# Kernel tuning notes

Hardware: AMD Instinct MI355X
Metric: run time of the kernel (lower is better)

## Reference

```python
import jax, jax.numpy as jnp
import numpy as np
from jax import lax

B, D, H, W = 8, 256, 56, 56
DH = 32            # d_head
HEADS = D // DH    # 8
WIN = 7            # window size
TOPK = 8           # top-k windows
DM = 4 * D         # mlp hidden = 1024
EPS = 1e-5


def bn(x, g, b, m, v):
    # inference-mode BatchNorm2d over channel dim of NCHW
    return g[:, None, None] * (x - m[:, None, None]) * lax.rsqrt(v[:, None, None] + EPS) + b[:, None, None]


def conv1x1(x, w):
    return jnp.einsum('bchw,oc->bohw', x, w)


def setup_inputs() -> dict:
    key = jax.random.key(0)
    ks = jax.random.split(key, 24)
    s = 0.05
    return {
        'x': jax.random.normal(ks[0], (B, D, H, W), jnp.float32),
        'g1': jax.random.uniform(ks[1], (D,)) + 0.5,
        'b1': jax.random.normal(ks[2], (D,)) * s,
        'm1': jax.random.normal(ks[3], (D,)) * s,
        'v1': jax.random.uniform(ks[4], (D,)) + 0.5,
        'W_qkv': jax.random.normal(ks[5], (3 * D, D)) * s,
        'W_merge': jax.random.normal(ks[6], (D, D)) * s,
        'b_merge': jax.random.normal(ks[7], (D,)) * s,
        'W1': jax.random.normal(ks[8], (DM, D)) * s,
        'g2': jax.random.uniform(ks[9], (DM,)) + 0.5,
        'b2': jax.random.normal(ks[10], (DM,)) * s,
        'm2': jax.random.normal(ks[11], (DM,)) * s,
        'v2': jax.random.uniform(ks[12], (DM,)) + 0.5,
        'Wdw': jax.random.normal(ks[13], (DM, 1, 3, 3)) * s,
        'g3': jax.random.uniform(ks[14], (DM,)) + 0.5,
        'b3': jax.random.normal(ks[15], (DM,)) * s,
        'm3': jax.random.normal(ks[16], (DM,)) * s,
        'v3': jax.random.uniform(ks[17], (DM,)) + 0.5,
        'W2': jax.random.normal(ks[18], (D, DM)) * s,
        'g4': jax.random.uniform(ks[19], (D,)) + 0.5,
        'b4': jax.random.normal(ks[20], (D,)) * s,
        'm4': jax.random.normal(ks[21], (D,)) * s,
        'v4': jax.random.uniform(ks[22], (D,)) + 0.5,
    }


def _forward(x, g1, b1, m1, v1, W_qkv, W_merge, b_merge,
             W1, g2, b2, m2, v2, Wdw, g3, b3, m3, v3, W2, g4, b4, m4, v4):
    b_, d, Hh, Ww = x.shape
    nh, nw = Hh // WIN, Ww // WIN
    nWnd, ww = nh * nw, WIN * WIN

    # qkv projection: BN -> GELU -> 1x1 conv
    h = jax.nn.gelu(bn(x, g1, b1, m1, v1), approximate=False)
    qkv = conv1x1(h, W_qkv)
    q, k, v = jnp.split(qkv, 3, axis=1)  # each [b, d, H, W]

    def part(t):  # -> [b, heads, nWnd, ww, dh]
        t = t.reshape(b_, HEADS, DH, nh, WIN, nw, WIN)
        return jnp.transpose(t, (0, 1, 3, 5, 4, 6, 2)).reshape(b_, HEADS, nWnd, ww, DH)

    qw, kw, vw = part(q), part(k), part(v)

    # window-level routing: mean-pooled q/k per window, top-k window selection
    def pool(t):  # [b, d, H, W] -> [b, nWnd, d]
        t = t.reshape(b_, d, nh, WIN, nw, WIN).mean(axis=(3, 5))
        return t.reshape(b_, d, nWnd).transpose(0, 2, 1)

    qr, kr = pool(q), pool(k)
    aff = jnp.einsum('bnd,bmd->bnm', qr, kr)        # [b, nWnd, nWnd]
    idx = lax.top_k(aff, TOPK)[1]                    # [b, nWnd, TOPK]

    def gath(t, i):  # t [heads, nWnd, ww, dh], i [nWnd, TOPK]
        return t[:, i]  # [heads, nWnd, TOPK, ww, dh]

    kg = jax.vmap(gath)(kw, idx).reshape(b_, HEADS, nWnd, TOPK * ww, DH)
    vg = jax.vmap(gath)(vw, idx).reshape(b_, HEADS, nWnd, TOPK * ww, DH)

    scores = jnp.einsum('bhnqd,bhnkd->bhnqk', qw, kg) / jnp.sqrt(jnp.float32(DH))
    attn = jax.nn.softmax(scores, axis=-1)
    out = jnp.einsum('bhnqk,bhnkd->bhnqd', attn, vg)  # [b, heads, nWnd, ww, dh]

    # un-partition back to [b, d, H, W]
    out = out.reshape(b_, HEADS, nh, nw, WIN, WIN, DH)
    msg = jnp.transpose(out, (0, 1, 6, 2, 4, 3, 5)).reshape(b_, d, Hh, Ww)

    # merge (1x1 conv with bias) + residual
    x = x + conv1x1(msg, W_merge) + b_merge[None, :, None, None]

    # MB mlp block: 1x1 -> BN -> GELU -> dw3x3 -> BN -> GELU -> 1x1 -> BN
    h2 = conv1x1(x, W1)
    h2 = jax.nn.gelu(bn(h2, g2, b2, m2, v2), approximate=False)
    h2 = lax.conv_general_dilated(h2, Wdw, (1, 1), 'SAME',
                                  feature_group_count=DM,
                                  dimension_numbers=('NCHW', 'OIHW', 'NCHW'))
    h2 = jax.nn.gelu(bn(h2, g3, b3, m3, v3), approximate=False)
    h2 = conv1x1(h2, W2)
    h2 = bn(h2, g4, b4, m4, v4)
    return x + h2


def reference(x, g1, b1, m1, v1, W_qkv, W_merge, b_merge,
              W1, g2, b2, m2, v2, Wdw, g3, b3, m3, v3, W2, g4, b4, m4, v4):
    return _forward(x, g1, b1, m1, v1, W_qkv, W_merge, b_merge,
                    W1, g2, b2, m2, v2, Wdw, g3, b3, m3, v3, W2, g4, b4, m4, v4)
```

## Files before the change

### kernel.cpp

```cpp
#include <hip/hip_runtime.h>
#include <cstdint>
#include <cstddef>

#define BB 8
#define PP 3136
#define EPSV 1e-5f
#define SCQK 0.17677669529663687f

using bf16x8 = __attribute__((ext_vector_type(8))) short;
using f32x4  = __attribute__((ext_vector_type(4))) float;

__device__ __forceinline__ float bf2f(unsigned short u) {
    union { float f; unsigned int i; } c; c.i = ((unsigned int)u) << 16; return c.f;
}
__device__ __forceinline__ unsigned short f2bf(float f) {
    union { float f; unsigned int i; } c; c.f = f;
    unsigned int r = c.i + 0x7FFFu + ((c.i >> 16) & 1u);
    return (unsigned short)(r >> 16);
}
__device__ __forceinline__ float gelu_f(float t) {
    return 0.5f * t * (1.0f + erff(t * 0.70710678118654752440f));
}
__device__ __forceinline__ float gelu_fast(float x) {
    float z = 1.5957691216057308f * (x + 0.044715f * x * x * x);
    return x / (1.0f + __expf(-z));
}
__device__ __forceinline__ void async16(const void* g, void* s) {
    __builtin_amdgcn_global_load_lds(
        (const __attribute__((address_space(1))) unsigned int*)g,
        (__attribute__((address_space(3))) unsigned int*)s, 16, 0, 0);
}
__device__ __forceinline__ uint4 pack8(const float* v) {
    uint4 o;
    o.x = (unsigned)f2bf(v[0]) | ((unsigned)f2bf(v[1]) << 16);
    o.y = (unsigned)f2bf(v[2]) | ((unsigned)f2bf(v[3]) << 16);
    o.z = (unsigned)f2bf(v[4]) | ((unsigned)f2bf(v[5]) << 16);
    o.w = (unsigned)f2bf(v[6]) | ((unsigned)f2bf(v[7]) << 16);
    return o;
}

__global__ __launch_bounds__(256) void cvt_all_k(
    const float* __restrict__ Wq, const float* __restrict__ Wm,
    const float* __restrict__ W1, const float* __restrict__ W2,
    unsigned short* __restrict__ dq, unsigned short* __restrict__ dm,
    unsigned short* __restrict__ d1, unsigned short* __restrict__ d2)
{
    int i = blockIdx.x * 256 + threadIdx.x;
    if (i < 196608) dq[i] = f2bf(Wq[i]);
    else if (i < 262144) dm[i - 196608] = f2bf(Wm[i - 196608]);
    else if (i < 524288) d1[i - 262144] = f2bf(W1[i - 262144]);
    else d2[i - 524288] = f2bf(W2[i - 524288]);
}

__global__ __launch_bounds__(256) void transin_k(const float* __restrict__ x,
    const float* __restrict__ g1, const float* __restrict__ b1,
    const float* __restrict__ m1, const float* __restrict__ v1,
    float* __restrict__ x_pm, unsigned short* __restrict__ h_bf)
{
    __shared__ float tile[64][65];
    __shared__ float gam[64], bet[64], mu[64], rst[64];
    const int p0 = blockIdx.x * 64, c0 = blockIdx.y * 64, b = blockIdx.z;
    const int t = threadIdx.x;
    if (t < 64) { int c = c0 + t; gam[t] = g1[c]; bet[t] = b1[c]; mu[t] = m1[c]; rst[t] = rsqrtf(v1[c] + EPSV); }
    {
        int cl = t >> 2, px = (t & 3) * 16;
        const float* src = x + ((size_t)(b * 256 + c0 + cl)) * PP + p0 + px;
        #pragma unroll
        for (int i4 = 0; i4 < 4; i4++) {
            float4 r0 = *(const float4*)(src + i4 * 4);
            tile[cl][px + i4*4 + 0] = r0.x; tile[cl][px + i4*4 + 1] = r0.y;
            tile[cl][px + i4*4 + 2] = r0.z; tile[cl][px + i4*4 + 3] = r0.w;
        }
    }
    __syncthreads();
    {
        int pl = t >> 2, cb = (t & 3) * 16;
        float raw[16], hg[16];
        #pragma unroll
        for (int i = 0; i < 16; i++) {
            float vv = tile[cb + i][pl];
            raw[i] = vv;
            hg[i] = gelu_fast(gam[cb + i] * (vv - mu[cb + i]) * rst[cb + i] + bet[cb + i]);
        }
        size_t off = ((size_t)b * PP + p0 + pl) * 256 + c0 + cb;
        float* xd = x_pm + off;
        #pragma unroll
        for (int i4 = 0; i4 < 4; i4++) {
            float4 o; o.x = raw[i4*4]; o.y = raw[i4*4+1]; o.z = raw[i4*4+2]; o.w = raw[i4*4+3];
            *(float4*)(xd + i4 * 4) = o;
        }
        uint4* hd = (uint4*)(h_bf + off);
        hd[0] = pack8(&hg[0]);
        hd[1] = pack8(&hg[8]);
    }
}

template<int EPI>
__global__ __launch_bounds__(256) void gemm_mfma_k(
    const unsigned short* __restrict__ Aact,
    const unsigned short* __restrict__ Wbf,
    const int K, const int Mout,
    void* __restrict__ C1, void* __restrict__ C2,
    const float* __restrict__ e0, const float* __restrict__ e1,
    const float* __restrict__ e2, const float* __restrict__ e3,
    const float* __restrict__ resid)
{
    __shared__ __align__(16) char smem[34816];
    unsigned short* As0 = (unsigned short*)smem;
    unsigned short* Bs0 = (unsigned short*)(smem + 16384);
    float* T = (float*)smem;

    const int tid = threadIdx.x;
    const int w = tid >> 6, lane = tid & 63, g = lane >> 4, l15 = lane & 15;
    const int wm = w >> 1, wn = w & 1;
    const size_t row0 = (size_t)blockIdx.x * 128;
    const int n0 = blockIdx.y * 128;
    const int srow = tid >> 2, scb = tid & 3;

    const f32x4 vzero = {0.f, 0.f, 0.f, 0.f};
    f32x4 acc[4][4];
    #pragma unroll
    for (int mf = 0; mf < 4; mf++)
        #pragma unroll
        for (int nf = 0; nf < 4; nf++) acc[mf][nf] = vzero;

    const int NT = K >> 5;

    auto STAGE = [&](int s) {
        const int k0 = s << 5;
        unsigned short* Ad = As0 + (s & 1) * 4096;
        unsigned short* Bd = Bs0 + (s & 1) * 4096;
        #pragma unroll
        for (int r = 0; r < 2; r++) {
            int row = r * 64 + srow;
            int cbp = scb ^ ((row >> 1) & 3);
            async16(Aact + (row0 + row) * K + k0 + cbp * 8, Ad + r * 2048 + w * 512);
            async16(Wbf + (size_t)(n0 + row) * K + k0 + cbp * 8, Bd + r * 2048 + w * 512);
        }
    };
    auto COMPUTE = [&](int t) {
        const unsigned short* Ab = As0 + (t & 1) * 4096;
        const unsigned short* Bb = Bs0 + (t & 1) * 4096;
        bf16x8 af[4], bfr[4];
        #pragma unroll
        for (int mf = 0; mf < 4; mf++) {
            int row = wm * 64 + mf * 16 + l15;
            int gb = g ^ ((row >> 1) & 3);
            af[mf] = *(const bf16x8*)&Ab[row * 32 + gb * 8];
        }
        #pragma unroll
        for (int nf = 0; nf < 4; nf++) {
            int row = wn * 64 + nf * 16 + l15;
            int gb = g ^ ((row >> 1) & 3);
            bfr[nf] = *(const bf16x8*)&Bb[row * 32 + gb * 8];
        }
        #pragma unroll
        for (int mf = 0; mf < 4; mf++)
            #pragma unroll
            for (int nf = 0; nf < 4; nf++)
                acc[mf][nf] = __builtin_amdgcn_mfma_f32_16x16x32_bf16(af[mf], bfr[nf], acc[mf][nf], 0, 0, 0);
    };

    STAGE(0);
    for (int t = 0; t < NT; ++t) {
        __syncthreads();
        if (t + 1 < NT) STAGE(t + 1);
        COMPUTE(t);
    }

    __syncthreads();
    const int erow = tid >> 1;
    const int ec0 = (tid & 1) * 32;
    #pragma unroll
    for (int pass = 0; pass < 2; ++pass) {
        if (pass) __syncthreads();
        if (wn == pass) {
            #pragma unroll
            for (int mf = 0; mf < 4; mf++)
                #pragma unroll
                for (int nf = 0; nf < 4; nf++)
                    #pragma unroll
                    for (int r = 0; r < 4; r++)
                        T[(wm * 64 + mf * 16 + g * 4 + r) * 68 + nf * 16 + l15] = acc[mf][nf][r];
        }
        __syncthreads();
        float vals[32];
        #pragma unroll
        for (int i = 0; i < 8; i++) {
            float4 v = *(const float4*)&T[erow * 68 + ec0 + i * 4];
            vals[i*4+0] = v.x; vals[i*4+1] = v.y; vals[i*4+2] = v.z; vals[i*4+3] = v.w;
        }
        const size_t prow = row0 + erow;
        const int mc0 = n0 + pass * 64 + ec0;
        const size_t off = prow * Mout + mc0;
        if (EPI == 0) {
            const float s = (mc0 < 256) ? SCQK : 1.0f;
            #pragma unroll
            for (int j = 0; j < 32; j++) vals[j] *= s;
            uint4* dst = (uint4*)((unsigned short*)C1 + off);
            #pragma unroll
            for (int i = 0; i < 4; i++) dst[i] = pack8(&vals[i * 8]);
        } else if (EPI == 1) {
            #pragma unroll
            for (int i = 0; i < 8; i++) {
                float4 bi = *(const float4*)(e0 + mc0 + i * 4);
                float4 rr = *(const float4*)(resid + off + i * 4);
                vals[i*4+0] += bi.x + rr.x; vals[i*4+1] += bi.y + rr.y;
                vals[i*4+2] += bi.z + rr.z; vals[i*4+3] += bi.w + rr.w;
            }
            float4* d1 = (float4*)((float*)C1 + off);
            #pragma unroll
            for (int i = 0; i < 8; i++) {
                float4 o; o.x = vals[i*4]; o.y = vals[i*4+1]; o.z = vals[i*4+2]; o.w = vals[i*4+3];
                d1[i] = o;
            }
            uint4* d2 = (uint4*)((unsigned short*)C2 + off);
            #pragma unroll
            for (int i = 0; i < 4; i++) d2[i] = pack8(&vals[i * 8]);
        } else if (EPI == 2) {
            #pragma unroll
            for (int i = 0; i < 8; i++) {
                float4 ga = *(const float4*)(e0 + mc0 + i * 4);
                float4 be = *(const float4*)(e1 + mc0 + i * 4);
                float4 mm = *(const float4*)(e2 + mc0 + i * 4);
                float4 vv = *(const float4*)(e3 + mc0 + i * 4);
                vals[i*4+0] = gelu_fast(ga.x * (vals[i*4+0] - mm.x) * rsqrtf(vv.x + EPSV) + be.x);
                vals[i*4+1] = gelu_fast(ga.y * (vals[i*4+1] - mm.y) * rsqrtf(vv.y + EPSV) + be.y);
                vals[i*4+2] = gelu_fast(ga.z * (vals[i*4+2] - mm.z) * rsqrtf(vv.z + EPSV) + be.z);
                vals[i*4+3] = gelu_fast(ga.w * (vals[i*4+3] - mm.w) * rsqrtf(vv.w + EPSV) + be.w);
            }
            uint4* dst = (uint4*)((unsigned short*)C1 + off);
            #pragma unroll
            for (int i = 0; i < 4; i++) dst[i] = pack8(&vals[i * 8]);
        } else {
            #pragma unroll
            for (int i = 0; i < 8; i++) {
                float4 ga = *(const float4*)(e0 + mc0 + i * 4);
                float4 be = *(const float4*)(e1 + mc0 + i * 4);
                float4 mm = *(const float4*)(e2 + mc0 + i * 4);
                float4 vv = *(const float4*)(e3 + mc0 + i * 4);
                float4 rr = *(const float4*)(resid + off + i * 4);
                vals[i*4+0] = ga.x * (vals[i*4+0] - mm.x) * rsqrtf(vv.x + EPSV) + be.x + rr.x;
                vals[i*4+1] = ga.y * (vals[i*4+1] - mm.y) * rsqrtf(vv.y + EPSV) + be.y + rr.y;
                vals[i*4+2] = ga.z * (vals[i*4+2] - mm.z) * rsqrtf(vv.z + EPSV) + be.z + rr.z;
                vals[i*4+3] = ga.w * (vals[i*4+3] - mm.w) * rsqrtf(vv.w + EPSV) + be.w + rr.w;
            }
            float4* d1 = (float4*)((float*)C1 + off);
            #pragma unroll
            for (int i = 0; i < 8; i++) {
                float4 o; o.x = vals[i*4]; o.y = vals[i*4+1]; o.z = vals[i*4+2]; o.w = vals[i*4+3];
                d1[i] = o;
            }
        }
    }
}

__global__ __launch_bounds__(256) void poolh_k(const float* __restrict__ x_pm,
    const float* __restrict__ g1, const float* __restrict__ b1,
    const float* __restrict__ m1, const float* __restrict__ v1,
    float* __restrict__ ph)
{
    __shared__ float part[4][256];
    __shared__ float gam[256], bet[256], mu[256], rst[256];
    const int n = blockIdx.x, b = blockIdx.y, t = threadIdx.x;
    gam[t] = g1[t]; bet[t] = b1[t]; mu[t] = m1[t]; rst[t] = rsqrtf(v1[t] + EPSV);
    __syncthreads();
    const int c4 = (t & 63) * 4, pg = t >> 6;
    float s0 = 0.f, s1 = 0.f, s2 = 0.f, s3 = 0.f;
    for (int j = pg; j < 49; j += 4) {
        int p = ((n >> 3) * 7 + j / 7) * 56 + (n & 7) * 7 + j % 7;
        float4 vx = *(const float4*)(x_pm + ((size_t)b * PP + p) * 256 + c4);
        s0 += gelu_f(gam[c4+0] * (vx.x - mu[c4+0]) * rst[c4+0] + bet[c4+0]);
        s1 += gelu_f(gam[c4+1] * (vx.y - mu[c4+1]) * rst[c4+1] + bet[c4+1]);
        s2 += gelu_f(gam[c4+2] * (vx.z - mu[c4+2]) * rst[c4+2] + bet[c4+2]);
        s3 += gelu_f(gam[c4+3] * (vx.w - mu[c4+3]) * rst[c4+3] + bet[c4+3]);
    }
    part[pg][c4 + 0] = s0; part[pg][c4 + 1] = s1; part[pg][c4 + 2] = s2; part[pg][c4 + 3] = s3;
    __syncthreads();
    float tot = part[0][t] + part[1][t] + part[2][t] + part[3][t];
    ph[((size_t)b * 64 + n) * 256 + t] = tot * (1.0f / 49.0f);
}

__global__ __launch_bounds__(256) void qrkr_k(const float* __restrict__ ph,
    const float* __restrict__ Wqkv, float* __restrict__ qr, float* __restrict__ kr)
{
    __shared__ float row[256];
    const int n = blockIdx.x, b = blockIdx.y, t = threadIdx.x;
    row[t] = ph[((size_t)b * 64 + n) * 256 + t];
    __syncthreads();
    const float* wq = Wqkv + (size_t)t * 256;
    const float* wk = Wqkv + (size_t)(256 + t) * 256;
    float aq = 0.f, ak = 0.f;
    #pragma unroll 4
    for (int k = 0; k < 256; k += 4) {
        float4 a4 = *(const float4*)(wq + k);
        float4 b4 = *(const float4*)(wk + k);
        aq += row[k]*a4.x + row[k+1]*a4.y + row[k+2]*a4.z + row[k+3]*a4.w;
        ak += row[k]*b4.x + row[k+1]*b4.y + row[k+2]*b4.z + row[k+3]*b4.w;
    }
    qr[((size_t)b * 64 + n) * 256 + t] = aq;
    kr[((size_t)b * 64 + n) * 256 + t] = ak;
}

__global__ __launch_bounds__(64) void topk_k(const float* __restrict__ qr,
    const float* __restrict__ kr, int* __restrict__ idxb)
{
    const int n = blockIdx.x, b_ = blockIdx.y;
    const int tid = threadIdx.x;
    __shared__ float qrow[256];
    *reinterpret_cast<float4*>(&qrow[tid * 4]) =
        *reinterpret_cast<const float4*>(qr + ((size_t)(b_ * 64) + n) * 256 + tid * 4);
    __syncthreads();
    const float* kp = kr + ((size_t)(b_ * 64) + tid) * 256;
    float av = 0.f;
    #pragma unroll 4
    for (int c = 0; c < 256; c++) av = fmaf(qrow[c], kp[c], av);
    for (int t = 0; t < 8; t++) {
        float v = av; int id = tid;
        #pragma unroll
        for (int off = 32; off; off >>= 1) {
            float v2 = __shfl_xor(v, off);
            int id2 = __shfl_xor(id, off);
            if (v2 > v || (v2 == v && id2 < id)) { v = v2; id = id2; }
        }
        if (tid == 0) idxb[((b_ * 64) + n) * 8 + t] = id;
        if (tid == id) av = -1e30f;
    }
}

__global__ __launch_bounds__(256) void attn_mfma_k(const unsigned short* __restrict__ qkv,
    const int* __restrict__ idxb, unsigned short* __restrict__ msg)
{
    __shared__ __align__(16) unsigned short Ks[64 * 40];
    __shared__ __align__(16) unsigned short Vt[32 * 72];
    __shared__ __align__(16) unsigned short Pr[4][16 * 72];
    const int n = blockIdx.x, h = blockIdx.y, b = blockIdx.z;
    const int tid = threadIdx.x;
    const int w = tid >> 6, lane = tid & 63, g = lane >> 4, l15 = lane & 15;

    for (int e = tid; e < 64 * 40; e += 256) Ks[e] = 0;
    for (int e = tid; e < 32 * 72; e += 256) Vt[e] = 0;

    const int iq = w * 16 + l15;
    bf16x8 qf = {0, 0, 0, 0, 0, 0, 0, 0};
    if (iq < 49) {
        int p = ((n >> 3) * 7 + iq / 7) * 56 + (n & 7) * 7 + iq % 7;
        qf = *(const bf16x8*)(qkv + ((size_t)b * PP + p) * 768 + h * 32 + g * 8);
    }
    const f32x4 vzero = {0.f, 0.f, 0.f, 0.f};
    f32x4 o0 = vzero, o1 = vzero;
    float mrow = -1e30f, lrow = 0.f;

    const bool act = tid < 196;
    const int jrow = tid >> 2, c8 = (tid & 3) * 8;
    uint4 kk_r = {0,0,0,0}, vv_r = {0,0,0,0};
    auto LOADW = [&](int t) {
        int wsrc = idxb[((b * 64) + n) * 8 + t];
        int p = ((wsrc >> 3) * 7 + jrow / 7) * 56 + (wsrc & 7) * 7 + jrow % 7;
        const unsigned short* srcp = qkv + ((size_t)b * PP + p) * 768 + 256 + h * 32 + c8;
        kk_r = *(const uint4*)srcp;
        vv_r = *(const uint4*)(srcp + 256);
    };
    if (act) LOADW(0);

    for (int t = 0; t < 8; t++) {
        __syncthreads();
        if (act) {
            *(uint4*)&Ks[jrow * 40 + c8] = kk_r;
            const unsigned short* pv = (const unsigned short*)&vv_r;
            #pragma unroll
            for (int jj = 0; jj < 8; jj++) {
                int dh = c8 + jj;
                Vt[dh * 72 + (jrow ^ (((dh >> 3) & 3) << 3))] = pv[jj];
            }
            if (t < 7) LOADW(t + 1);
        }
        __syncthreads();
        f32x4 s[4];
        #pragma unroll
        for (int nf = 0; nf < 4; nf++) {
            bf16x8 kf = *(const bf16x8*)&Ks[(nf * 16 + l15) * 40 + g * 8];
            s[nf] = __builtin_amdgcn_mfma_f32_16x16x32_bf16(kf, qf, vzero, 0, 0, 0);
        }
        float sv[16];
        #pragma unroll
        for (int nf = 0; nf < 4; nf++)
            #pragma unroll
            for (int r = 0; r < 4; r++) {
                int j = nf * 16 + g * 4 + r;
                sv[nf * 4 + r] = (j < 49) ? s[nf][r] : -1e30f;
            }
        float wmx = sv[0];
        #pragma unroll
        for (int e = 1; e < 16; e++) wmx = fmaxf(wmx, sv[e]);
        wmx = fmaxf(wmx, __shfl_xor(wmx, 16));
        wmx = fmaxf(wmx, __shfl_xor(wmx, 32));
        float mn = fmaxf(mrow, wmx);
        float corr = __expf(mrow - mn);
        mrow = mn;
        float rsum = 0.f;
        #pragma unroll
        for (int e = 0; e < 16; e++) { float pe = __expf(sv[e] - mn); sv[e] = pe; rsum += pe; }
        rsum += __shfl_xor(rsum, 16);
        rsum += __shfl_xor(rsum, 32);
        lrow = lrow * corr + rsum;
        #pragma unroll
        for (int r = 0; r < 4; r++) { o0[r] *= corr; o1[r] *= corr; }
        #pragma unroll
        for (int nf = 0; nf < 4; nf++) {
            uint2 pw;
            pw.x = (unsigned)f2bf(sv[nf*4+0]) | ((unsigned)f2bf(sv[nf*4+1]) << 16);
            pw.y = (unsigned)f2bf(sv[nf*4+2]) | ((unsigned)f2bf(sv[nf*4+3]) << 16);
            *(uint2*)&Pr[w][l15 * 72 + nf * 16 + g * 4] = pw;
        }
        asm volatile("s_waitcnt lgkmcnt(0)" ::: "memory");
        #pragma unroll
        for (int ks = 0; ks < 2; ks++) {
            const int j0 = ks * 32 + g * 8;
            bf16x8 pf  = *(const bf16x8*)&Pr[w][l15 * 72 + j0];
            bf16x8 vf0 = *(const bf16x8*)&Vt[l15 * 72 + (j0 ^ (((l15 >> 3) & 1) << 3))];
            bf16x8 vf1 = *(const bf16x8*)&Vt[(16 + l15) * 72 + (j0 ^ ((2 + (l15 >> 3)) << 3))];
            o0 = __builtin_amdgcn_mfma_f32_16x16x32_bf16(vf0, pf, o0, 0, 0, 0);
            o1 = __builtin_amdgcn_mfma_f32_16x16x32_bf16(vf1, pf, o1, 0, 0, 0);
        }
    }
    if (iq < 49) {
        float inv = 1.0f / lrow;
        int p = ((n >> 3) * 7 + iq / 7) * 56 + (n & 7) * 7 + iq % 7;
        size_t off = ((size_t)b * PP + p) * 256 + h * 32;
        uint2 w0, w1;
        w0.x = (unsigned)f2bf(o0[0]*inv) | ((unsigned)f2bf(o0[1]*inv) << 16);
        w0.y = (unsigned)f2bf(o0[2]*inv) | ((unsigned)f2bf(o0[3]*inv) << 16);
        w1.x = (unsigned)f2bf(o1[0]*inv) | ((unsigned)f2bf(o1[1]*inv) << 16);
        w1.y = (unsigned)f2bf(o1[2]*inv) | ((unsigned)f2bf(o1[3]*inv) << 16);
        *(uint2*)(msg + off + g * 4) = w0;
        *(uint2*)(msg + off + 16 + g * 4) = w1;
    }
}

__global__ __launch_bounds__(256) void dwconv_k(const unsigned short* __restrict__ in,
    const float* __restrict__ w9,
    const float* __restrict__ g3, const float* __restrict__ b3,
    const float* __restrict__ m3, const float* __restrict__ v3,
    unsigned short* __restrict__ out)
{
    __shared__ __align__(16) unsigned short tl[100 * 64];
    const int sx = blockIdx.x % 7, sy = blockIdx.x / 7;
    const int c0 = blockIdx.y * 64, b = blockIdx.z;
    const int t = threadIdx.x;
    for (int e = t; e < 800; e += 256) {
        int pos = e >> 3, c8 = (e & 7) * 8;
        int iy = sy * 8 + pos / 10 - 1, ix = sx * 8 + pos % 10 - 1;
        uint4 val = {0u, 0u, 0u, 0u};
        if (iy >= 0 && iy < 56 && ix >= 0 && ix < 56)
            val = *(const uint4*)(in + ((size_t)b * PP + iy * 56 + ix) * 1024 + c0 + c8);
        *(uint4*)&tl[pos * 64 + c8] = val;
    }
    __syncthreads();
    const int c2 = (t & 31) * 2, pg = t >> 5;
    const int c = c0 + c2;
    float w0[9], w1[9];
    #pragma unroll
    for (int i = 0; i < 9; i++) { w0[i] = w9[c * 9 + i]; w1[i] = w9[(c + 1) * 9 + i]; }
    const float ga0 = g3[c], be0 = b3[c], mu0 = m3[c], rs0 = rsqrtf(v3[c] + EPSV);
    const float ga1 = g3[c+1], be1 = b3[c+1], mu1 = m3[c+1], rs1 = rsqrtf(v3[c+1] + EPSV);
    #pragma unroll
    for (int q = 0; q < 8; q++) {
        int pos = pg * 8 + q, y = pos >> 3, xq = pos & 7;
        float s0 = 0.f, s1 = 0.f;
        #pragma unroll
        for (int dy = 0; dy < 3; dy++)
            #pragma unroll
            for (int dx = 0; dx < 3; dx++) {
                unsigned int u = *(const unsigned int*)&tl[((y + dy) * 10 + xq + dx) * 64 + c2];
                s0 = fmaf(bf2f((unsigned short)(u & 0xffffu)), w0[dy * 3 + dx], s0);
                s1 = fmaf(bf2f((unsigned short)(u >> 16)), w1[dy * 3 + dx], s1);
            }
        float y0 = gelu_fast(ga0 * (s0 - mu0) * rs0 + be0);
        float y1 = gelu_fast(ga1 * (s1 - mu1) * rs1 + be1);
        unsigned int ow = (unsigned int)f2bf(y0) | ((unsigned int)f2bf(y1) << 16);
        size_t off = ((size_t)b * PP + (sy * 8 + y) * 56 + sx * 8 + xq) * 1024 + c;
        *(unsigned int*)&out[off] = ow;
    }
}

__global__ __launch_bounds__(256) void transout_k(const float* __restrict__ out_pm,
    float* __restrict__ dout)
{
    __shared__ float tile[64][65];
    const int p0 = blockIdx.x * 64, c0 = blockIdx.y * 64, b = blockIdx.z;
    const int t = threadIdx.x;
    {
        int pl = t >> 2, cx = (t & 3) * 16;
        const float* src = out_pm + ((size_t)b * PP + p0 + pl) * 256 + c0 + cx;
        #pragma unroll
        for (int i4 = 0; i4 < 4; i4++) {
            float4 vv = *(const float4*)(src + i4 * 4);
            tile[pl][cx + i4*4 + 0] = vv.x; tile[pl][cx + i4*4 + 1] = vv.y;
            tile[pl][cx + i4*4 + 2] = vv.z; tile[pl][cx + i4*4 + 3] = vv.w;
        }
    }
    __syncthreads();
    {
        int cl = t >> 2, px = (t & 3) * 16;
        float* dst = dout + ((size_t)(b * 256 + c0 + cl)) * PP + p0 + px;
        #pragma unroll
        for (int i4 = 0; i4 < 4; i4++) {
            float4 o;
            o.x = tile[px + i4*4 + 0][cl]; o.y = tile[px + i4*4 + 1][cl];
            o.z = tile[px + i4*4 + 2][cl]; o.w = tile[px + i4*4 + 3][cl];
            *(float4*)(dst + i4 * 4) = o;
        }
    }
}

extern "C" void kernel_launch(void* const* d_in, const int* in_sizes, int n_in,
                              void* d_out, int out_size, void* d_ws, size_t ws_size,
                              hipStream_t stream)
{
    const float* x      = (const float*)d_in[0];
    const float* g1     = (const float*)d_in[1];
    const float* b1     = (const float*)d_in[2];
    const float* m1     = (const float*)d_in[3];
    const float* v1     = (const float*)d_in[4];
    const float* Wqkv   = (const float*)d_in[5];
    const float* Wmerge = (const float*)d_in[6];
    const float* bmerge = (const float*)d_in[7];
    const float* W1     = (const float*)d_in[8];
    const float* g2     = (const float*)d_in[9];
    const float* b2     = (const float*)d_in[10];
    const float* m2     = (const float*)d_in[11];
    const float* v2     = (const float*)d_in[12];
    const float* Wdw    = (const float*)d_in[13];
    const float* g3     = (const float*)d_in[14];
    const float* b3     = (const float*)d_in[15];
    const float* m3     = (const float*)d_in[16];
    const float* v3     = (const float*)d_in[17];
    const float* W2     = (const float*)d_in[18];
    const float* g4     = (const float*)d_in[19];
    const float* b4     = (const float*)d_in[20];
    const float* m4     = (const float*)d_in[21];
    const float* v4     = (const float*)d_in[22];

    char* ws = (char*)d_ws;
    float*          x_pm   = (float*)(ws + 0);
    float*          x2_pm  = (float*)(ws + 25690112);
    unsigned short* x2_bf  = (unsigned short*)(ws + 51380224);
    unsigned short* qkv_pm = (unsigned short*)(ws + 64225280);
    unsigned short* msg_pm = (unsigned short*)(ws + 102760448);
    unsigned short* t1     = (unsigned short*)(ws + 115605504);
    unsigned short* h_bf   = t1;
    unsigned short* t2     = (unsigned short*)(ws + 166985728);
    float*          ph     = (float*)(ws + 218365952);
    float*          qr     = (float*)(ws + 218890240);
    float*          kr     = (float*)(ws + 219414528);
    int*            idxb   = (int*)(ws + 219938816);
    unsigned short* Wqkv_b = (unsigned short*)(ws + 219955200);
    unsigned short* Wmrg_b = (unsigned short*)(ws + 220348416);
    unsigned short* W1_b   = (unsigned short*)(ws + 220479488);
    unsigned short* W2_b   = (unsigned short*)(ws + 221003776);
    float*          out_pm = x_pm;
    if (ws_size < 221528064) return;

    cvt_all_k<<<3072, 256, 0, stream>>>(Wqkv, Wmerge, W1, W2, Wqkv_b, Wmrg_b, W1_b, W2_b);
    transin_k<<<dim3(49, 4, BB), 256, 0, stream>>>(x, g1, b1, m1, v1, x_pm, h_bf);
    gemm_mfma_k<0><<<dim3(196, 6), 256, 0, stream>>>(h_bf, Wqkv_b, 256, 768,
        qkv_pm, nullptr, nullptr, nullptr, nullptr, nullptr, nullptr);
    poolh_k<<<dim3(64, BB), 256, 0, stream>>>(x_pm, g1, b1, m1, v1, ph);
    qrkr_k<<<dim3(64, BB), 256, 0, stream>>>(ph, Wqkv, qr, kr);
    topk_k<<<dim3(64, BB), 64, 0, stream>>>(qr, kr, idxb);
    attn_mfma_k<<<dim3(64, 8, BB), 256, 0, stream>>>(qkv_pm, idxb, msg_pm);
    gemm_mfma_k<1><<<dim3(196, 2), 256, 0, stream>>>(msg_pm, Wmrg_b, 256, 256,
        x2_pm, x2_bf, bmerge, nullptr, nullptr, nullptr, x_pm);
    gemm_mfma_k<2><<<dim3(196, 8), 256, 0, stream>>>(x2_bf, W1_b, 256, 1024,
        t1, nullptr, g2, b2, m2, v2, nullptr);
    dwconv_k<<<dim3(49, 16, BB), 256, 0, stream>>>(t1, Wdw, g3, b3, m3, v3, t2);
    gemm_mfma_k<3><<<dim3(196, 2), 256, 0, stream>>>(t2, W2_b, 1024, 256,
        out_pm, nullptr, g4, b4, m4, v4, x2_pm);
    transout_k<<<dim3(49, 4, BB), 256, 0, stream>>>(out_pm, (float*)d_out);
}
```

Before: 340.9 us.

## Restructure GEMM to stream A from global, stage weights in LDS; load K directly

```diff
diff --git a/kernel.cpp b/kernel.cpp
--- a/kernel.cpp
+++ b/kernel.cpp
@@ -105,104 +105,97 @@
     const float* __restrict__ e2, const float* __restrict__ e3,
     const float* __restrict__ resid)
 {
-    __shared__ __align__(16) char smem[34816];
-    unsigned short* As0 = (unsigned short*)smem;
-    unsigned short* Bs0 = (unsigned short*)(smem + 16384);
+    __shared__ __align__(16) char smem[32768];
+    unsigned short* Bs = (unsigned short*)smem;
     float* T = (float*)smem;
 
     const int tid = threadIdx.x;
     const int w = tid >> 6, lane = tid & 63, g = lane >> 4, l15 = lane & 15;
     const int wm = w >> 1, wn = w & 1;
     const size_t row0 = (size_t)blockIdx.x * 128;
-    const int n0 = blockIdx.y * 128;
-    const int srow = tid >> 2, scb = tid & 3;
+    const int n0 = blockIdx.y * 64;
 
     const f32x4 vzero = {0.f, 0.f, 0.f, 0.f};
-    f32x4 acc[4][4];
+    f32x4 acc[4][2];
     #pragma unroll
     for (int mf = 0; mf < 4; mf++)
         #pragma unroll
-        for (int nf = 0; nf < 4; nf++) acc[mf][nf] = vzero;
-
-    const int NT = K >> 5;
-
-    auto STAGE = [&](int s) {
-        const int k0 = s << 5;
-        unsigned short* Ad = As0 + (s & 1) * 4096;
-        unsigned short* Bd = Bs0 + (s & 1) * 4096;
-        #pragma unroll
-        for (int r = 0; r < 2; r++) {
-            int row = r * 64 + srow;
-            int cbp = scb ^ ((row >> 1) & 3);
-            async16(Aact + (row0 + row) * K + k0 + cbp * 8, Ad + r * 2048 + w * 512);
-            async16(Wbf + (size_t)(n0 + row) * K + k0 + cbp * 8, Bd + r * 2048 + w * 512);
-        }
-    };
-    auto COMPUTE = [&](int t) {
-        const unsigned short* Ab = As0 + (t & 1) * 4096;
-        const unsigned short* Bb = Bs0 + (t & 1) * 4096;
-        bf16x8 af[4], bfr[4];
-        #pragma unroll
-        for (int mf = 0; mf < 4; mf++) {
-            int row = wm * 64 + mf * 16 + l15;
-            int gb = g ^ ((row >> 1) & 3);
-            af[mf] = *(const bf16x8*)&Ab[row * 32 + gb * 8];
-        }
-        #pragma unroll
-        for (int nf = 0; nf < 4; nf++) {
-            int row = wn * 64 + nf * 16 + l15;
-            int gb = g ^ ((row >> 1) & 3);
-            bfr[nf] = *(const bf16x8*)&Bb[row * 32 + gb * 8];
-        }
-        #pragma unroll
-        for (int mf = 0; mf < 4; mf++)
-            #pragma unroll
-            for (int nf = 0; nf < 4; nf++)
-                acc[mf][nf] = __builtin_amdgcn_mfma_f32_16x16x32_bf16(af[mf], bfr[nf], acc[mf][nf], 0, 0, 0);
-    };
-
-    STAGE(0);
-    for (int t = 0; t < NT; ++t) {
+        for (int nf = 0; nf < 2; nf++) acc[mf][nf] = vzero;
+
+    const int nchunk = K >> 8;
+    const unsigned short* Arow[4];
+    #pragma unroll
+    for (int mf = 0; mf < 4; mf++)
+        Arow[mf] = Aact + (row0 + wm * 64 + mf * 16 + l15) * (size_t)K + g * 8;
+
+    for (int c = 0; c < nchunk; ++c) {
+        if (c) __syncthreads();
+        #pragma unroll
+        for (int rd = 0; rd < 8; rd++) {
+            int idx = rd * 256 + tid;
+            int brow = idx >> 5;
+            int bcb  = idx & 31;
+            int bcbs = bcb ^ (brow & 15);
+            unsigned short* dst = Bs + ((rd * 256 + (tid & ~63)) << 3);
+            async16(Wbf + ((size_t)(n0 + brow)) * K + c * 256 + bcbs * 8, dst);
+        }
         __syncthreads();
-        if (t + 1 < NT) STAGE(t + 1);
-        COMPUTE(t);
-    }
-
-    __syncthreads();
-    const int erow = tid >> 1;
-    const int ec0 = (tid & 1) * 32;
-    #pragma unroll
-    for (int pass = 0; pass < 2; ++pass) {
-        if (pass) __syncthreads();
-        if (wn == pass) {
+        const int kc = c << 8;
+        #pragma unroll
+        for (int ks = 0; ks < 8; ks++) {
+            bf16x8 af[4];
+            #pragma unroll
+            for (int mf = 0; mf < 4; mf++)
+                af[mf] = *(const bf16x8*)(Arow[mf] + kc + ks * 32);
+            bf16x8 bfr[2];
+            #pragma unroll
+            for (int nf = 0; nf < 2; nf++) {
+                int brow = wn * 32 + nf * 16 + l15;
+                int bcb = (ks * 4 + g) ^ (brow & 15);
+                bfr[nf] = *(const bf16x8*)&Bs[brow * 256 + bcb * 8];
+            }
             #pragma unroll
             for (int mf = 0; mf < 4; mf++)
                 #pragma unroll
-                for (int nf = 0; nf < 4; nf++)
+                for (int nf = 0; nf < 2; nf++)
+                    acc[mf][nf] = __builtin_amdgcn_mfma_f32_16x16x32_bf16(af[mf], bfr[nf], acc[mf][nf], 0, 0, 0);
+        }
+    }
+
+    __syncthreads();
+    const int erow = tid >> 2;
+    const int ec0 = (tid & 3) * 16;
+    #pragma unroll
+    for (int half = 0; half < 2; ++half) {
+        if (half) __syncthreads();
+        if (wm == half) {
+            #pragma unroll
+            for (int mf = 0; mf < 4; mf++)
+                #pragma unroll
+                for (int nf = 0; nf < 2; nf++)
                     #pragma unroll
                     for (int r = 0; r < 4; r++)
-                        T[(wm * 64 + mf * 16 + g * 4 + r) * 68 + nf * 16 + l15] = acc[mf][nf][r];
+                        T[(mf * 16 + g * 4 + r) * 68 + wn * 32 + nf * 16 + l15] = acc[mf][nf][r];
         }
         __syncthreads();
-        float vals[32];
-        #pragma unroll
-        for (int i = 0; i < 8; i++) {
+        float vals[16];
+        #pragma unroll
+        for (int i = 0; i < 4; i++) {
             float4 v = *(const float4*)&T[erow * 68 + ec0 + i * 4];
             vals[i*4+0] = v.x; vals[i*4+1] = v.y; vals[i*4+2] = v.z; vals[i*4+3] = v.w;
         }
-        const size_t prow = row0 + erow;
-        const int mc0 = n0 + pass * 64 + ec0;
+        const size_t prow = row0 + half * 64 + erow;
+        const int mc0 = n0 + ec0;
         const size_t off = prow * Mout + mc0;
         if (EPI == 0) {
             const float s = (mc0 < 256) ? SCQK : 1.0f;
             #pragma unroll
-            for (int j = 0; j < 32; j++) vals[j] *= s;
+            for (int j = 0; j < 16; j++) vals[j] *= s;
             uint4* dst = (uint4*)((unsigned short*)C1 + off);
-            #pragma unroll
-            for (int i = 0; i < 4; i++) dst[i] = pack8(&vals[i * 8]);
+            dst[0] = pack8(&vals[0]); dst[1] = pack8(&vals[8]);
         } else if (EPI == 1) {
             #pragma unroll
-            for (int i = 0; i < 8; i++) {
+            for (int i = 0; i < 4; i++) {
                 float4 bi = *(const float4*)(e0 + mc0 + i * 4);
                 float4 rr = *(const float4*)(resid + off + i * 4);
                 vals[i*4+0] += bi.x + rr.x; vals[i*4+1] += bi.y + rr.y;
@@ -210,16 +203,15 @@
             }
             float4* d1 = (float4*)((float*)C1 + off);
             #pragma unroll
-            for (int i = 0; i < 8; i++) {
+            for (int i = 0; i < 4; i++) {
                 float4 o; o.x = vals[i*4]; o.y = vals[i*4+1]; o.z = vals[i*4+2]; o.w = vals[i*4+3];
                 d1[i] = o;
             }
             uint4* d2 = (uint4*)((unsigned short*)C2 + off);
-            #pragma unroll
-            for (int i = 0; i < 4; i++) d2[i] = pack8(&vals[i * 8]);
+            d2[0] = pack8(&vals[0]); d2[1] = pack8(&vals[8]);
         } else if (EPI == 2) {
             #pragma unroll
-            for (int i = 0; i < 8; i++) {
+            for (int i = 0; i < 4; i++) {
                 float4 ga = *(const float4*)(e0 + mc0 + i * 4);
                 float4 be = *(const float4*)(e1 + mc0 + i * 4);
                 float4 mm = *(const float4*)(e2 + mc0 + i * 4);
@@ -230,11 +222,10 @@
                 vals[i*4+3] = gelu_fast(ga.w * (vals[i*4+3] - mm.w) * rsqrtf(vv.w + EPSV) + be.w);
             }
             uint4* dst = (uint4*)((unsigned short*)C1 + off);
-            #pragma unroll
-            for (int i = 0; i < 4; i++) dst[i] = pack8(&vals[i * 8]);
+            dst[0] = pack8(&vals[0]); dst[1] = pack8(&vals[8]);
         } else {
             #pragma unroll
-            for (int i = 0; i < 8; i++) {
+            for (int i = 0; i < 4; i++) {
                 float4 ga = *(const float4*)(e0 + mc0 + i * 4);
                 float4 be = *(const float4*)(e1 + mc0 + i * 4);
                 float4 mm = *(const float4*)(e2 + mc0 + i * 4);
@@ -247,7 +238,7 @@
             }
             float4* d1 = (float4*)((float*)C1 + off);
             #pragma unroll
-            for (int i = 0; i < 8; i++) {
+            for (int i = 0; i < 4; i++) {
                 float4 o; o.x = vals[i*4]; o.y = vals[i*4+1]; o.z = vals[i*4+2]; o.w = vals[i*4+3];
                 d1[i] = o;
             }
@@ -331,14 +322,12 @@
 __global__ __launch_bounds__(256) void attn_mfma_k(const unsigned short* __restrict__ qkv,
     const int* __restrict__ idxb, unsigned short* __restrict__ msg)
 {
-    __shared__ __align__(16) unsigned short Ks[64 * 40];
     __shared__ __align__(16) unsigned short Vt[32 * 72];
     __shared__ __align__(16) unsigned short Pr[4][16 * 72];
     const int n = blockIdx.x, h = blockIdx.y, b = blockIdx.z;
     const int tid = threadIdx.x;
     const int w = tid >> 6, lane = tid & 63, g = lane >> 4, l15 = lane & 15;
 
-    for (int e = tid; e < 64 * 40; e += 256) Ks[e] = 0;
     for (int e = tid; e < 32 * 72; e += 256) Vt[e] = 0;
 
     const int iq = w * 16 + l15;
@@ -347,41 +336,52 @@
         int p = ((n >> 3) * 7 + iq / 7) * 56 + (n & 7) * 7 + iq % 7;
         qf = *(const bf16x8*)(qkv + ((size_t)b * PP + p) * 768 + h * 32 + g * 8);
     }
+    int widx[8];
+    {
+        const int* ip = idxb + ((b * 64) + n) * 8;
+        #pragma unroll
+        for (int t = 0; t < 8; t++) widx[t] = ip[t];
+    }
     const f32x4 vzero = {0.f, 0.f, 0.f, 0.f};
     f32x4 o0 = vzero, o1 = vzero;
     float mrow = -1e30f, lrow = 0.f;
 
     const bool act = tid < 196;
     const int jrow = tid >> 2, c8 = (tid & 3) * 8;
-    uint4 kk_r = {0,0,0,0}, vv_r = {0,0,0,0};
-    auto LOADW = [&](int t) {
-        int wsrc = idxb[((b * 64) + n) * 8 + t];
+    uint4 vv_r = {0,0,0,0};
+    auto LOADV = [&](int t) {
+        int wsrc = widx[t];
         int p = ((wsrc >> 3) * 7 + jrow / 7) * 56 + (wsrc & 7) * 7 + jrow % 7;
-        const unsigned short* srcp = qkv + ((size_t)b * PP + p) * 768 + 256 + h * 32 + c8;
-        kk_r = *(const uint4*)srcp;
-        vv_r = *(const uint4*)(srcp + 256);
+        vv_r = *(const uint4*)(qkv + ((size_t)b * PP + p) * 768 + 512 + h * 32 + c8);
     };
-    if (act) LOADW(0);
+    if (act) LOADV(0);
 
     for (int t = 0; t < 8; t++) {
+        const int wsrc = widx[t];
+        const int sy0 = (wsrc >> 3) * 7, sx0 = (wsrc & 7) * 7;
+        bf16x8 kf[4];
+        #pragma unroll
+        for (int nf = 0; nf < 4; nf++) {
+            int j = nf * 16 + l15;
+            int jc = (j < 49) ? j : 0;
+            int p = (sy0 + jc / 7) * 56 + sx0 + jc % 7;
+            kf[nf] = *(const bf16x8*)(qkv + ((size_t)b * PP + p) * 768 + 256 + h * 32 + g * 8);
+        }
         __syncthreads();
         if (act) {
-            *(uint4*)&Ks[jrow * 40 + c8] = kk_r;
             const unsigned short* pv = (const unsigned short*)&vv_r;
             #pragma unroll
             for (int jj = 0; jj < 8; jj++) {
                 int dh = c8 + jj;
                 Vt[dh * 72 + (jrow ^ (((dh >> 3) & 3) << 3))] = pv[jj];
             }
-            if (t < 7) LOADW(t + 1);
+            if (t < 7) LOADV(t + 1);
         }
         __syncthreads();
         f32x4 s[4];
         #pragma unroll
-        for (int nf = 0; nf < 4; nf++) {
-            bf16x8 kf = *(const bf16x8*)&Ks[(nf * 16 + l15) * 40 + g * 8];
-            s[nf] = __builtin_amdgcn_mfma_f32_16x16x32_bf16(kf, qf, vzero, 0, 0, 0);
-        }
+        for (int nf = 0; nf < 4; nf++)
+            s[nf] = __builtin_amdgcn_mfma_f32_16x16x32_bf16(kf[nf], qf, vzero, 0, 0, 0);
         float sv[16];
         #pragma unroll
         for (int nf = 0; nf < 4; nf++)
@@ -564,18 +564,18 @@
 
     cvt_all_k<<<3072, 256, 0, stream>>>(Wqkv, Wmerge, W1, W2, Wqkv_b, Wmrg_b, W1_b, W2_b);
     transin_k<<<dim3(49, 4, BB), 256, 0, stream>>>(x, g1, b1, m1, v1, x_pm, h_bf);
-    gemm_mfma_k<0><<<dim3(196, 6), 256, 0, stream>>>(h_bf, Wqkv_b, 256, 768,
+    gemm_mfma_k<0><<<dim3(196, 12), 256, 0, stream>>>(h_bf, Wqkv_b, 256, 768,
         qkv_pm, nullptr, nullptr, nullptr, nullptr, nullptr, nullptr);
     poolh_k<<<dim3(64, BB), 256, 0, stream>>>(x_pm, g1, b1, m1, v1, ph);
     qrkr_k<<<dim3(64, BB), 256, 0, stream>>>(ph, Wqkv, qr, kr);
     topk_k<<<dim3(64, BB), 64, 0, stream>>>(qr, kr, idxb);
     attn_mfma_k<<<dim3(64, 8, BB), 256, 0, stream>>>(qkv_pm, idxb, msg_pm);
-    gemm_mfma_k<1><<<dim3(196, 2), 256, 0, stream>>>(msg_pm, Wmrg_b, 256, 256,
+    gemm_mfma_k<1><<<dim3(196, 4), 256, 0, stream>>>(msg_pm, Wmrg_b, 256, 256,
         x2_pm, x2_bf, bmerge, nullptr, nullptr, nullptr, x_pm);
-    gemm_mfma_k<2><<<dim3(196, 8), 256, 0, stream>>>(x2_bf, W1_b, 256, 1024,
+    gemm_mfma_k<2><<<dim3(196, 16), 256, 0, stream>>>(x2_bf, W1_b, 256, 1024,
         t1, nullptr, g2, b2, m2, v2, nullptr);
     dwconv_k<<<dim3(49, 16, BB), 256, 0, stream>>>(t1, Wdw, g3, b3, m3, v3, t2);
-    gemm_mfma_k<3><<<dim3(196, 2), 256, 0, stream>>>(t2, W2_b, 1024, 256,
+    gemm_mfma_k<3><<<dim3(196, 4), 256, 0, stream>>>(t2, W2_b, 1024, 256,
         out_pm, nullptr, g4, b4, m4, v4, x2_pm);
     transout_k<<<dim3(49, 4, BB), 256, 0, stream>>>(out_pm, (float*)d_out);
 }
```

New measurement: 440.5 us. 1.29x slower.
